# Kernel optimization log

Measured on AMD Instinct MI355X. Metric: run time of the kernel, lower is better.

Reference implementation:

```python
import jax, jax.numpy as jnp
import numpy as np

D = 1024      # embed_dim
H = 16        # num_heads
HD = D // H   # head_dim


def setup_inputs() -> dict:
    key = jax.random.key(0)
    ks = jax.random.split(key, 9)
    s = 0.02
    x = jax.random.normal(ks[0], (8, 1024, D), dtype=jnp.float32)
    # Per-head Q/K/V linears, torch Linear layout [out, in] -> stacked [H, HD, D]
    Wq = jax.random.normal(ks[1], (H, HD, D), dtype=jnp.float32) * s
    Wk = jax.random.normal(ks[2], (H, HD, D), dtype=jnp.float32) * s
    Wv = jax.random.normal(ks[3], (H, HD, D), dtype=jnp.float32) * s
    bq = jax.random.normal(ks[4], (H, HD), dtype=jnp.float32) * s
    bk = jax.random.normal(ks[5], (H, HD), dtype=jnp.float32) * s
    bv = jax.random.normal(ks[6], (H, HD), dtype=jnp.float32) * s
    Wo = jax.random.normal(ks[7], (D, D), dtype=jnp.float32) * s
    bo = jax.random.normal(ks[8], (D,), dtype=jnp.float32) * s
    return {"x": x, "Wq": Wq, "Wk": Wk, "Wv": Wv,
            "bq": bq, "bk": bk, "bv": bv, "Wo": Wo, "bo": bo}


def reference(x, Wq, Wk, Wv, bq, bk, bv, Wo, bo):
    # Batched per-head projections: [B,S,D] x [H,HD,D] -> [B,H,S,HD]
    q = jnp.einsum('bsd,hkd->bhsk', x, Wq) + bq[None, :, None, :]
    k = jnp.einsum('bsd,hkd->bhsk', x, Wk) + bk[None, :, None, :]
    v = jnp.einsum('bsd,hkd->bhsk', x, Wv) + bv[None, :, None, :]
    scores = jnp.einsum('bhqk,bhsk->bhqs', q, k) / jnp.sqrt(jnp.float32(HD))
    probs = jax.nn.softmax(scores, axis=-1)          # [B,H,S,S]
    attn = jnp.einsum('bhqs,bhsk->bhqk', probs, v)   # [B,H,S,HD]
    # Concat heads along feature dim -> [B,S,D]
    B, _, S, _ = attn.shape
    concat = jnp.transpose(attn, (0, 2, 1, 3)).reshape(B, S, D)
    out = jnp.einsum('bsd,ed->bse', concat, Wo) + bo  # output projection
    return out
```

## Files before the change

kernel.cpp:

```cpp
#include <hip/hip_runtime.h>
#include <stdint.h>
#include <stddef.h>


typedef short bf16x8 __attribute__((ext_vector_type(8)));
typedef float f32x4  __attribute__((ext_vector_type(4)));
typedef unsigned short u16x8 __attribute__((ext_vector_type(8)));
typedef unsigned short u16x4 __attribute__((ext_vector_type(4)));

#define MFMA16 __builtin_amdgcn_mfma_f32_16x16x32_bf16

typedef const void __attribute__((address_space(1)))* gas1_t;
typedef void __attribute__((address_space(3)))* las3_t;

static __device__ __forceinline__ void gload16(const void* g, void* l) {
  __builtin_amdgcn_global_load_lds((gas1_t)g, (las3_t)l, 16, 0, 0);
}

static __device__ __forceinline__ unsigned short f2bf(float f) {
  union { float f; unsigned int u; } v; v.f = f;
  unsigned int r = v.u + 0x7fffu + ((v.u >> 16) & 1u);
  return (unsigned short)(r >> 16);
}

__global__ __launch_bounds__(256) void cast_all(
    const float* __restrict__ x, const float* __restrict__ Wq,
    const float* __restrict__ Wk, const float* __restrict__ Wv,
    const float* __restrict__ Wo,
    unsigned short* __restrict__ xb, unsigned short* __restrict__ wqkv,
    unsigned short* __restrict__ wob) {
  int base = (blockIdx.x * 256 + threadIdx.x) * 4;
  const float* s; unsigned short* d;
  if (base < 8388608) { s = x + base; d = xb + base; }
  else if (base < 11534336) {
    int o = base - 8388608; int wi = o >> 20;
    const float* w = (wi == 0) ? Wq : (wi == 1) ? Wk : Wv;
    s = w + (o & 1048575); d = wqkv + o;
  } else {
    int o = base - 11534336; s = Wo + o; d = wob + o;
  }
  float4 f = *(const float4*)s;
  u16x4 r; r[0] = f2bf(f.x); r[1] = f2bf(f.y); r[2] = f2bf(f.z); r[3] = f2bf(f.w);
  *(u16x4*)d = r;
}

template <int EPI, int NBX, bool SWZ>
__global__ __launch_bounds__(256) void gemm128(
    const unsigned short* __restrict__ A, const unsigned short* __restrict__ Bm,
    float* __restrict__ Cf, const float* __restrict__ bO,
    unsigned short* __restrict__ Qo, unsigned short* __restrict__ Ko,
    unsigned short* __restrict__ Vo,
    const float* __restrict__ bq, const float* __restrict__ bk,
    const float* __restrict__ bv) {
  __shared__ __align__(16) char sm[65536];
  const int tid = threadIdx.x, lane = tid & 63, w = tid >> 6;
  const int wr = w >> 1, wc = w & 1;
  int i = blockIdx.x, j;
  if constexpr (SWZ) j = (i & 7) * (NBX * 64 / 8) + (i >> 3);
  else j = i;
  const int bcol = (j % NBX) * 128, brow = (j / NBX) * 128;
  const int l15 = lane & 15, g = lane >> 4;

  auto stage = [&](int ks, int buf) {
    char* Ad = sm + buf * 32768;
    char* Bd = Ad + 16384;
#pragma unroll
    for (int jj = 0; jj < 4; ++jj) {
      int p = (w * 4 + jj) * 1024 + lane * 16;
      int row = p >> 7;
      int cl = (lane & 7) ^ (row & 7);
      gload16(A + (size_t)(brow + row) * 1024 + ks * 64 + cl * 8,
              Ad + (w * 4 + jj) * 1024);
      gload16(Bm + (size_t)(bcol + row) * 1024 + ks * 64 + cl * 8,
              Bd + (w * 4 + jj) * 1024);
    }
  };

  stage(0, 0);
  asm volatile("s_waitcnt vmcnt(0)" ::: "memory");
  __syncthreads();

  f32x4 acc[4][4] = {};
  for (int ks = 0; ks < 16; ++ks) {
    const int cur = ks & 1;
    if (ks < 15) stage(ks + 1, cur ^ 1);
    const char* As = sm + cur * 32768;
    const char* Bs = As + 16384;
#pragma unroll
    for (int kk = 0; kk < 2; ++kk) {
      bf16x8 af[4], bfr[4];
#pragma unroll
      for (int mi = 0; mi < 4; ++mi) {
        int row = wr * 64 + mi * 16 + l15;
        int off = (row * 128 + kk * 64 + g * 16) ^ ((row & 7) << 4);
        af[mi] = *(const bf16x8*)(As + off);
      }
#pragma unroll
      for (int ni = 0; ni < 4; ++ni) {
        int row = wc * 64 + ni * 16 + l15;
        int off = (row * 128 + kk * 64 + g * 16) ^ ((row & 7) << 4);
        bfr[ni] = *(const bf16x8*)(Bs + off);
      }
#pragma unroll
      for (int mi = 0; mi < 4; ++mi)
#pragma unroll
        for (int ni = 0; ni < 4; ++ni)
          acc[mi][ni] = MFMA16(af[mi], bfr[ni], acc[mi][ni], 0, 0, 0);
    }
    asm volatile("s_waitcnt vmcnt(0)" ::: "memory");
    __syncthreads();
  }
  if constexpr (EPI == 0) {
    const int b = brow >> 10;
#pragma unroll
    for (int ni = 0; ni < 4; ++ni) {
      int n = bcol + wc * 64 + ni * 16 + l15;
      int t = n >> 10, nh = n & 1023;
      int h = nh >> 6, hd = nh & 63;
      const float* bias = (t == 0) ? bq : (t == 1) ? bk : bv;
      float bb = bias[nh];
      if (t == 2) {
        size_t vtb = ((size_t)(b * 16 + h) * 64 + hd) * 1024;
#pragma unroll
        for (int mi = 0; mi < 4; ++mi) {
          int m0 = brow + wr * 64 + mi * 16 + g * 4;
          int srow0 = m0 & 1023;
          u16x4 vv;
#pragma unroll
          for (int r = 0; r < 4; ++r) vv[r] = f2bf(acc[mi][ni][r] + bb);
          *(u16x4*)(Vo + vtb + srow0) = vv;
        }
      } else {
        float scale = (t == 0) ? 0.125f : 1.0f;
        unsigned short* dst = (t == 0) ? Qo : Ko;
        size_t basei = ((size_t)(b * 16 + h) * 1024) * 64 + hd;
#pragma unroll
        for (int mi = 0; mi < 4; ++mi)
#pragma unroll
          for (int r = 0; r < 4; ++r) {
            int m = brow + wr * 64 + mi * 16 + g * 4 + r;
            int srow = m & 1023;
            dst[basei + (size_t)srow * 64] = f2bf((acc[mi][ni][r] + bb) * scale);
          }
      }
    }
  } else {
#pragma unroll
    for (int ni = 0; ni < 4; ++ni) {
      int n = bcol + wc * 64 + ni * 16 + l15;
      float bb = bO[n];
#pragma unroll
      for (int mi = 0; mi < 4; ++mi)
#pragma unroll
        for (int r = 0; r < 4; ++r) {
          int m = brow + wr * 64 + mi * 16 + g * 4 + r;
          Cf[(size_t)m * 1024 + n] = acc[mi][ni][r] + bb;
        }
    }
  }
}

__global__ __launch_bounds__(256, 3) void attn_fused(
    const unsigned short* __restrict__ Qb, const unsigned short* __restrict__ Kb,
    const unsigned short* __restrict__ VtG, unsigned short* __restrict__ Cc) {
  __shared__ __align__(16) char sm[49152];
  char* Ks = sm;
  char* Vt = sm + 16384;
  const int tid = threadIdx.x, lane = tid & 63, w = tid >> 6;
  char* Ps = sm + 32768 + w * 4096;
  const int l15 = lane & 15, g = lane >> 4;
  const int id = blockIdx.x;
  const int qt = id >> 7, bh = id & 127;
  const size_t hb = (size_t)bh * (1024 * 64);

  bf16x8 qreg[2][2];
#pragma unroll
  for (int kk = 0; kk < 2; ++kk)
#pragma unroll
    for (int ni = 0; ni < 2; ++ni) {
      int q = qt * 128 + w * 32 + ni * 16 + l15;
      qreg[kk][ni] = *(const bf16x8*)(Qb + hb + (size_t)q * 64 + kk * 32 + g * 8);
    }

  auto stage = [&](int c, int buf) {
#pragma unroll
    for (int j = 0; j < 2; ++j) {
      int p = (w * 2 + j) * 1024 + lane * 16;
      int row = p >> 7;
      int cl = (lane & 7) ^ (row & 7);
      gload16(Kb + hb + (size_t)(c * 64 + row) * 64 + cl * 8,
              Ks + buf * 8192 + (w * 2 + j) * 1024);
      gload16(VtG + hb + (size_t)row * 1024 + c * 64 + cl * 8,
              Vt + buf * 8192 + (w * 2 + j) * 1024);
    }
  };

  stage(0, 0);
  asm volatile("s_waitcnt vmcnt(0)" ::: "memory");
  __syncthreads();

  f32x4 acc[4][2] = {};
  float m_run[2] = {-1e30f, -1e30f};
  float l_run[2] = {0.f, 0.f};

  for (int c = 0; c < 16; ++c) {
    const int cur = c & 1;
    if (c < 15) stage(c + 1, cur ^ 1);
    const char* Kc = Ks + cur * 8192;
    const char* Vc = Vt + cur * 8192;

    f32x4 st[4][2] = {};
#pragma unroll
    for (int kk = 0; kk < 2; ++kk) {
      bf16x8 ka[4];
#pragma unroll
      for (int mi = 0; mi < 4; ++mi) {
        int row = mi * 16 + l15;
        int off = (row * 128 + kk * 64 + g * 16) ^ ((row & 7) << 4);
        ka[mi] = *(const bf16x8*)(Kc + off);
      }
#pragma unroll
      for (int mi = 0; mi < 4; ++mi)
#pragma unroll
        for (int ni = 0; ni < 2; ++ni)
          st[mi][ni] = MFMA16(ka[mi], qreg[kk][ni], st[mi][ni], 0, 0, 0);
    }

    float corr_s[2];
#pragma unroll
    for (int ni = 0; ni < 2; ++ni) {
      float mx = -1e30f;
#pragma unroll
      for (int mi = 0; mi < 4; ++mi)
#pragma unroll
        for (int r = 0; r < 4; ++r) mx = fmaxf(mx, st[mi][ni][r]);
      mx = fmaxf(mx, __shfl_xor(mx, 16));
      mx = fmaxf(mx, __shfl_xor(mx, 32));
      float mn = fmaxf(m_run[ni], mx);
      float corr = __expf(m_run[ni] - mn);
      float sum = 0.f;
      const int q = ni * 16 + l15;
      const int rbase = q * 128, sw = (q & 7) << 4;
#pragma unroll
      for (int mi = 0; mi < 4; ++mi) {
        u16x4 pk;
#pragma unroll
        for (int r = 0; r < 4; ++r) {
          float e = __expf(st[mi][ni][r] - mn);
          sum += e;
          pk[r] = f2bf(e);
        }
        *(u16x4*)(Ps + ((rbase + (mi * 16 + g * 4) * 2) ^ sw)) = pk;
      }
      sum += __shfl_xor(sum, 16);
      sum += __shfl_xor(sum, 32);
      l_run[ni] = l_run[ni] * corr + sum;
      m_run[ni] = mn;
      corr_s[ni] = corr;
    }

#pragma unroll
    for (int nd = 0; nd < 4; ++nd)
#pragma unroll
      for (int ni = 0; ni < 2; ++ni)
#pragma unroll
        for (int r = 0; r < 4; ++r)
          acc[nd][ni][r] *= corr_s[ni];

#pragma unroll
    for (int kk = 0; kk < 2; ++kk) {
      bf16x8 vf[4], pa[2];
#pragma unroll
      for (int nd = 0; nd < 4; ++nd) {
        int row = nd * 16 + l15;
        int off = (row * 128 + kk * 64 + g * 16) ^ ((row & 7) << 4);
        vf[nd] = *(const bf16x8*)(Vc + off);
      }
#pragma unroll
      for (int ni = 0; ni < 2; ++ni) {
        int q = ni * 16 + l15;
        int off = (q * 128 + kk * 64 + g * 16) ^ ((q & 7) << 4);
        pa[ni] = *(const bf16x8*)(Ps + off);
      }
#pragma unroll
      for (int nd = 0; nd < 4; ++nd)
#pragma unroll
        for (int ni = 0; ni < 2; ++ni)
          acc[nd][ni] = MFMA16(vf[nd], pa[ni], acc[nd][ni], 0, 0, 0);
    }

    asm volatile("s_waitcnt vmcnt(0)" ::: "memory");
    __syncthreads();
  }

  const int b = bh >> 4, h = bh & 15;
  float invl[2] = {1.f / l_run[0], 1.f / l_run[1]};
#pragma unroll
  for (int ni = 0; ni < 2; ++ni) {
    int q = qt * 128 + w * 32 + ni * 16 + l15;
    size_t rowb = (size_t)(b * 1024 + q) * 1024 + h * 64;
#pragma unroll
    for (int nd = 0; nd < 4; ++nd) {
      u16x4 o;
#pragma unroll
      for (int r = 0; r < 4; ++r) o[r] = f2bf(acc[nd][ni][r] * invl[ni]);
      *(u16x4*)(Cc + rowb + nd * 16 + g * 4) = o;
    }
  }
}

extern "C" void kernel_launch(void* const* d_in, const int* in_sizes, int n_in,
                              void* d_out, int out_size, void* d_ws, size_t ws_size,
                              hipStream_t stream) {
  const float* x  = (const float*)d_in[0];
  const float* Wq = (const float*)d_in[1];
  const float* Wk = (const float*)d_in[2];
  const float* Wv = (const float*)d_in[3];
  const float* bq = (const float*)d_in[4];
  const float* bk = (const float*)d_in[5];
  const float* bv = (const float*)d_in[6];
  const float* Wo = (const float*)d_in[7];
  const float* bo = (const float*)d_in[8];

  char* ws = (char*)d_ws;
  unsigned short* xb   = (unsigned short*)(ws);
  unsigned short* wqkv = (unsigned short*)(ws + 16777216);
  unsigned short* wob  = (unsigned short*)(ws + 23068672);
  unsigned short* Qb   = (unsigned short*)(ws + 25165824);
  unsigned short* Kb   = (unsigned short*)(ws + 41943040);
  unsigned short* VtG  = (unsigned short*)(ws + 58720256);
  unsigned short* Cc   = xb;

  cast_all<<<dim3(12288), dim3(256), 0, stream>>>(x, Wq, Wk, Wv, Wo, xb, wqkv, wob);
  gemm128<0, 24, true><<<dim3(1536), dim3(256), 0, stream>>>(
      xb, wqkv, nullptr, nullptr, Qb, Kb, VtG, bq, bk, bv);
  attn_fused<<<dim3(1024), dim3(256), 0, stream>>>(Qb, Kb, VtG, Cc);
  gemm128<1, 8, false><<<dim3(512), dim3(256), 0, stream>>>(
      Cc, wob, (float*)d_out, bo, nullptr, nullptr, nullptr, nullptr, nullptr, nullptr);
}
```

Before: 252.6 us.

## Use 256x256 tile, 8-wave QKV GEMM with phased prefetch pipeline

Replaces the 128x128 templated GEMM used for the QKV projection with a dedicated 256x256-tile kernel that runs 512 threads and 128KB of shared memory. Global-to-LDS loads for the next k-tile are spread across four compute phases, with barriers and s_setprio raised around the MFMA bursts. The larger tile is meant to raise arithmetic intensity and cut redundant operand loads. It gives up the grid swizzle and brings only 384 blocks, so occupancy and tail balance could suffer. The output GEMM is split into its own non-templated kernel with the same behaviour as before.

```diff
diff --git a/kernel.cpp b/kernel.cpp
--- a/kernel.cpp
+++ b/kernel.cpp
@@ -44,21 +44,128 @@
   *(u16x4*)d = r;
 }
 
-template <int EPI, int NBX, bool SWZ>
-__global__ __launch_bounds__(256) void gemm128(
-    const unsigned short* __restrict__ A, const unsigned short* __restrict__ Bm,
-    float* __restrict__ Cf, const float* __restrict__ bO,
+__global__ __launch_bounds__(512, 2) void gemm256_qkv(
+    const unsigned short* __restrict__ Ag, const unsigned short* __restrict__ Bg,
     unsigned short* __restrict__ Qo, unsigned short* __restrict__ Ko,
     unsigned short* __restrict__ Vo,
     const float* __restrict__ bq, const float* __restrict__ bk,
     const float* __restrict__ bv) {
+  __shared__ __align__(16) char sm[131072];
+  const int tid = threadIdx.x, lane = tid & 63, w = tid >> 6;
+  const int wr = w >> 2, wc = w & 3;
+  const int l15 = lane & 15, g = lane >> 4;
+  const int bcol = blockIdx.x * 256, brow = blockIdx.y * 256;
+
+  auto stage2 = [&](int kt, int buf, int p) {
+#pragma unroll
+    for (int jj = 0; jj < 2; ++jj) {
+      int rowBase, region;
+      const unsigned short* src;
+      if (p < 2) {
+        int j = p * 2 + jj;
+        rowBase = wr * 128 + wc * 32 + j * 8;
+        region = 0; src = Ag + (size_t)(brow + rowBase) * 1024;
+      } else {
+        int j = (p - 2) * 2 + jj;
+        rowBase = (wc >> 1) * 128 + (wr * 2 + (wc & 1)) * 32 + j * 8;
+        region = 32768; src = Bg + (size_t)(bcol + rowBase) * 1024;
+      }
+      int rlo = lane >> 3;
+      int cl = (lane & 7) ^ ((rowBase + rlo) & 7);
+      gload16(src + (size_t)rlo * 1024 + kt * 64 + cl * 8,
+              sm + buf * 65536 + region + rowBase * 128);
+    }
+  };
+
+#pragma unroll
+  for (int p = 0; p < 4; ++p) stage2(0, 0, p);
+  asm volatile("s_waitcnt vmcnt(0)" ::: "memory");
+  __builtin_amdgcn_s_barrier();
+
+  f32x4 acc[8][4] = {};
+  bf16x8 bfr[4];
+  for (int t = 0; t < 16; ++t) {
+    const int cur = t & 1;
+    const char* As = sm + cur * 65536;
+    const char* Bs = As + 32768;
+#pragma unroll
+    for (int ph = 0; ph < 4; ++ph) {
+      const int qm = ph & 1, kk = ph >> 1;
+      if (qm == 0) {
+#pragma unroll
+        for (int nc = 0; nc < 4; ++nc) {
+          int row = wc * 64 + nc * 16 + l15;
+          int off = (row * 128 + kk * 64 + g * 16) ^ ((row & 7) << 4);
+          bfr[nc] = *(const bf16x8*)(Bs + off);
+        }
+      }
+      bf16x8 af[4];
+#pragma unroll
+      for (int mr = 0; mr < 4; ++mr) {
+        int row = wr * 128 + qm * 64 + mr * 16 + l15;
+        int off = (row * 128 + kk * 64 + g * 16) ^ ((row & 7) << 4);
+        af[mr] = *(const bf16x8*)(As + off);
+      }
+      if (t < 15) stage2(t + 1, cur ^ 1, ph);
+      __builtin_amdgcn_s_barrier();
+      __builtin_amdgcn_s_setprio(1);
+#pragma unroll
+      for (int mr = 0; mr < 4; ++mr)
+#pragma unroll
+        for (int nc = 0; nc < 4; ++nc)
+          acc[qm * 4 + mr][nc] = MFMA16(af[mr], bfr[nc], acc[qm * 4 + mr][nc], 0, 0, 0);
+      __builtin_amdgcn_s_setprio(0);
+      if (ph == 3)
+        asm volatile("s_waitcnt vmcnt(0)" ::: "memory");
+      __builtin_amdgcn_s_barrier();
+    }
+  }
+
+  const int bb_ = brow >> 10;
+#pragma unroll
+  for (int nc = 0; nc < 4; ++nc) {
+    int n = bcol + wc * 64 + nc * 16 + l15;
+    int tt = n >> 10, nh = n & 1023;
+    int h = nh >> 6, hd = nh & 63;
+    const float* bias = (tt == 0) ? bq : (tt == 1) ? bk : bv;
+    float bbv = bias[nh];
+    if (tt == 2) {
+      size_t vtb = ((size_t)(bb_ * 16 + h) * 64 + hd) * 1024;
+#pragma unroll
+      for (int qm = 0; qm < 2; ++qm)
+#pragma unroll
+        for (int mr = 0; mr < 4; ++mr) {
+          int m0 = brow + wr * 128 + qm * 64 + mr * 16 + g * 4;
+          int srow0 = m0 & 1023;
+          u16x4 vv;
+#pragma unroll
+          for (int r = 0; r < 4; ++r) vv[r] = f2bf(acc[qm * 4 + mr][nc][r] + bbv);
+          *(u16x4*)(Vo + vtb + srow0) = vv;
+        }
+    } else {
+      float scale = (tt == 0) ? 0.125f : 1.0f;
+      unsigned short* dst = (tt == 0) ? Qo : Ko;
+      size_t basei = ((size_t)(bb_ * 16 + h) * 1024) * 64 + hd;
+#pragma unroll
+      for (int qm = 0; qm < 2; ++qm)
+#pragma unroll
+        for (int mr = 0; mr < 4; ++mr)
+#pragma unroll
+          for (int r = 0; r < 4; ++r) {
+            int m = brow + wr * 128 + qm * 64 + mr * 16 + g * 4 + r;
+            dst[basei + (size_t)(m & 1023) * 64] = f2bf((acc[qm * 4 + mr][nc][r] + bbv) * scale);
+          }
+    }
+  }
+}
+
+__global__ __launch_bounds__(256) void gemm128_out(
+    const unsigned short* __restrict__ A, const unsigned short* __restrict__ Bm,
+    float* __restrict__ Cf, const float* __restrict__ bO) {
   __shared__ __align__(16) char sm[65536];
   const int tid = threadIdx.x, lane = tid & 63, w = tid >> 6;
   const int wr = w >> 1, wc = w & 1;
-  int i = blockIdx.x, j;
-  if constexpr (SWZ) j = (i & 7) * (NBX * 64 / 8) + (i >> 3);
-  else j = i;
-  const int bcol = (j % NBX) * 128, brow = (j / NBX) * 128;
+  const int bcol = (blockIdx.x & 7) * 128, brow = (blockIdx.x >> 3) * 128;
   const int l15 = lane & 15, g = lane >> 4;
 
   auto stage = [&](int ks, int buf) {
@@ -110,53 +217,17 @@
     asm volatile("s_waitcnt vmcnt(0)" ::: "memory");
     __syncthreads();
   }
-  if constexpr (EPI == 0) {
-    const int b = brow >> 10;
-#pragma unroll
-    for (int ni = 0; ni < 4; ++ni) {
-      int n = bcol + wc * 64 + ni * 16 + l15;
-      int t = n >> 10, nh = n & 1023;
-      int h = nh >> 6, hd = nh & 63;
-      const float* bias = (t == 0) ? bq : (t == 1) ? bk : bv;
-      float bb = bias[nh];
-      if (t == 2) {
-        size_t vtb = ((size_t)(b * 16 + h) * 64 + hd) * 1024;
-#pragma unroll
-        for (int mi = 0; mi < 4; ++mi) {
-          int m0 = brow + wr * 64 + mi * 16 + g * 4;
-          int srow0 = m0 & 1023;
-          u16x4 vv;
-#pragma unroll
-          for (int r = 0; r < 4; ++r) vv[r] = f2bf(acc[mi][ni][r] + bb);
-          *(u16x4*)(Vo + vtb + srow0) = vv;
-        }
-      } else {
-        float scale = (t == 0) ? 0.125f : 1.0f;
-        unsigned short* dst = (t == 0) ? Qo : Ko;
-        size_t basei = ((size_t)(b * 16 + h) * 1024) * 64 + hd;
-#pragma unroll
-        for (int mi = 0; mi < 4; ++mi)
-#pragma unroll
-          for (int r = 0; r < 4; ++r) {
-            int m = brow + wr * 64 + mi * 16 + g * 4 + r;
-            int srow = m & 1023;
-            dst[basei + (size_t)srow * 64] = f2bf((acc[mi][ni][r] + bb) * scale);
-          }
-      }
-    }
-  } else {
-#pragma unroll
-    for (int ni = 0; ni < 4; ++ni) {
-      int n = bcol + wc * 64 + ni * 16 + l15;
-      float bb = bO[n];
-#pragma unroll
-      for (int mi = 0; mi < 4; ++mi)
-#pragma unroll
-        for (int r = 0; r < 4; ++r) {
-          int m = brow + wr * 64 + mi * 16 + g * 4 + r;
-          Cf[(size_t)m * 1024 + n] = acc[mi][ni][r] + bb;
-        }
-    }
+#pragma unroll
+  for (int ni = 0; ni < 4; ++ni) {
+    int n = bcol + wc * 64 + ni * 16 + l15;
+    float bb = bO[n];
+#pragma unroll
+    for (int mi = 0; mi < 4; ++mi)
+#pragma unroll
+      for (int r = 0; r < 4; ++r) {
+        int m = brow + wr * 64 + mi * 16 + g * 4 + r;
+        Cf[(size_t)m * 1024 + n] = acc[mi][ni][r] + bb;
+      }
   }
 }
 
@@ -332,9 +403,8 @@
   unsigned short* Cc   = xb;
 
   cast_all<<<dim3(12288), dim3(256), 0, stream>>>(x, Wq, Wk, Wv, Wo, xb, wqkv, wob);
-  gemm128<0, 24, true><<<dim3(1536), dim3(256), 0, stream>>>(
-      xb, wqkv, nullptr, nullptr, Qb, Kb, VtG, bq, bk, bv);
+  gemm256_qkv<<<dim3(12, 32), dim3(512), 0, stream>>>(
+      xb, wqkv, Qb, Kb, VtG, bq, bk, bv);
   attn_fused<<<dim3(1024), dim3(256), 0, stream>>>(Qb, Kb, VtG, Cc);
-  gemm128<1, 8, false><<<dim3(512), dim3(256), 0, stream>>>(
-      Cc, wob, (float*)d_out, bo, nullptr, nullptr, nullptr, nullptr, nullptr, nullptr);
-}
+  gemm128_out<<<dim3(512), dim3(256), 0, stream>>>(Cc, wob, (float*)d_out, bo);
+}
```

Result: slower. 261.7 us (+3.6%).
